# Optimization experiments

Hardware: AMD Instinct MI355X
Metric: run time of the kernel (lower is better)

Reference implementation:

```python
import jax, jax.numpy as jnp
import numpy as np

H = 8  # n_head

def rel_shift(x):
    # x: [B, H, S, 2S-1] -> [B, H, S, S]
    B, h, S, _ = x.shape
    x_padded = jnp.pad(x, ((0, 0), (0, 0), (0, 0), (1, 0)))  # [B,H,S,2S]
    x_padded = x_padded.reshape(B, h, 2 * S, S)
    x = x_padded[:, :, 1:, :].reshape(B, h, S, 2 * S - 1)
    return x[:, :, :, :S]

def setup_inputs() -> dict:
    key = jax.random.key(0)
    ks = jax.random.split(key, 16)
    B, S, D = 8, 1024, 512
    C = D // H
    inp = {
        "query": jax.random.normal(ks[0], (B, S, D), jnp.float32),
        "key": jax.random.normal(ks[1], (B, S, D), jnp.float32),
        "value": jax.random.normal(ks[2], (B, S, D), jnp.float32),
        "pos_emb": jax.random.normal(ks[3], (1, 2 * S - 1, D), jnp.float32),
        "mask": jnp.zeros((B, S), dtype=bool),
        "Wq": jax.random.normal(ks[4], (D, D), jnp.float32) / np.sqrt(D),
        "bq": jnp.zeros((D,), jnp.float32),
        "Wk": jax.random.normal(ks[5], (D, D), jnp.float32) / np.sqrt(D),
        "bk": jnp.zeros((D,), jnp.float32),
        "Wv": jax.random.normal(ks[6], (D, D), jnp.float32) / np.sqrt(D),
        "bv": jnp.zeros((D,), jnp.float32),
        "Wpos": jax.random.normal(ks[7], (D, D), jnp.float32) / np.sqrt(D),
        "Wout": jax.random.normal(ks[8], (D, D), jnp.float32) / np.sqrt(D),
        "bout": jnp.zeros((D,), jnp.float32),
        "u_bias": jax.random.normal(ks[9], (H, C), jnp.float32) / np.sqrt(C),
        "v_bias": jax.random.normal(ks[10], (H, C), jnp.float32) / np.sqrt(C),
    }
    return inp

def reference(query, key, value, pos_emb, mask, Wq, bq, Wk, bk, Wv, bv,
              Wpos, Wout, bout, u_bias, v_bias):
    B, S, D = query.shape
    C = D // H
    # qkv projections -> [B, H, S, C]
    q = (query @ Wq + bq).reshape(B, S, H, C).transpose(0, 2, 1, 3)
    k = (key @ Wk + bk).reshape(B, S, H, C).transpose(0, 2, 1, 3)
    v = (value @ Wv + bv).reshape(B, S, H, C).transpose(0, 2, 1, 3)
    # positional projection: pos_emb [1, 2S-1, D] -> p [H, 2S-1, C]
    P = pos_emb.shape[1]
    p = (pos_emb[0] @ Wpos).reshape(P, H, C).transpose(1, 0, 2)
    q_u = q + u_bias[:, None, :]
    q_v = q + v_bias[:, None, :]
    matrix_ac = jnp.einsum('bhsc,bhtc->bhst', q_u, k)           # [B,H,S,S]
    matrix_bd = jnp.einsum('bhsc,htc->bhst', q_v, p)            # [B,H,S,2S-1]
    matrix_bd = rel_shift(matrix_bd)                            # [B,H,S,S]
    scores = (matrix_ac + matrix_bd) / jnp.sqrt(jnp.float32(C))
    scores = jnp.where(mask[:, None, None, :], -jnp.inf, scores)
    p_attn = jax.nn.softmax(scores, axis=-1)
    x = jnp.einsum('bhst,bhtc->bhsc', p_attn, v)
    x = x.transpose(0, 2, 1, 3).reshape(B, S, D)
    return x @ Wout + bout
```

## Files before the change

### kernel.cpp

```cpp
#include <hip/hip_runtime.h>
#include <math.h>

typedef unsigned short ushort_t;
typedef __attribute__((ext_vector_type(8))) short short8;
typedef __attribute__((ext_vector_type(4))) float f32x4;

#define MFMA(a,b,c) __builtin_amdgcn_mfma_f32_16x16x32_bf16((a),(b),(c),0,0,0)

#define BB 8
#define SS 1024
#define DD 512
#define HH 8
#define CC 64
#define PP 2047

static __device__ __forceinline__ ushort_t f2bf(float f) {
    unsigned u = __float_as_uint(f);
    u += 0x7fffu + ((u >> 16) & 1u);
    return (ushort_t)(u >> 16);
}
static __device__ __forceinline__ unsigned pack2(float a, float b) {
    return (unsigned)f2bf(a) | ((unsigned)f2bf(b) << 16);
}

__global__ __launch_bounds__(256) void wtrans_kernel(
    const float* __restrict__ Wq, const float* __restrict__ Wk,
    const float* __restrict__ Wv, const float* __restrict__ Wp,
    const float* __restrict__ Wo, ushort_t* __restrict__ wt)
{
    __shared__ float T[64][65];
    const int bid = blockIdx.x, tid = threadIdx.x;
    const int wi   = bid >> 6;
    const int tile = bid & 63;
    const float* Wsrc = (wi == 0) ? Wq : (wi == 1) ? Wk : (wi == 2) ? Wv
                      : (wi == 3) ? Wp : Wo;
    ushort_t* Wdst = wt + (size_t)wi * 262144;
    const int tk0 = (tile >> 3) * 64, tn0 = (tile & 7) * 64;
    const int r = tid >> 2, c4 = (tid & 3) * 16;
    #pragma unroll
    for (int rep = 0; rep < 4; ++rep) {
        float4 f = *(const float4*)(Wsrc + (size_t)(tk0 + r) * 512 + tn0 + c4 + rep * 4);
        T[r][c4 + rep * 4 + 0] = f.x; T[r][c4 + rep * 4 + 1] = f.y;
        T[r][c4 + rep * 4 + 2] = f.z; T[r][c4 + rep * 4 + 3] = f.w;
    }
    __syncthreads();
    #pragma unroll
    for (int rep = 0; rep < 4; ++rep) {
        uint2 u;
        u.x = pack2(T[c4 + rep * 4 + 0][r], T[c4 + rep * 4 + 1][r]);
        u.y = pack2(T[c4 + rep * 4 + 2][r], T[c4 + rep * 4 + 3][r]);
        *(uint2*)(Wdst + (size_t)(tn0 + r) * 512 + tk0 + c4 + rep * 4) = u;
    }
}

__global__ __launch_bounds__(256) void qkvpos_kernel(
    const float* __restrict__ Xq, const float* __restrict__ Xk,
    const float* __restrict__ Xv, const float* __restrict__ Xp,
    const ushort_t* __restrict__ wt,
    const float* __restrict__ bq, const float* __restrict__ bk,
    const float* __restrict__ bv,
    const float* __restrict__ ub, const float* __restrict__ vbias,
    ushort_t* __restrict__ qu, ushort_t* __restrict__ qvo,
    ushort_t* __restrict__ kbuf, ushort_t* __restrict__ vtb,
    ushort_t* __restrict__ pbuf)
{
    __shared__ __align__(16) ushort_t Xs[128][72];
    __shared__ __align__(16) ushort_t Ws[128][72];
    const int tid = threadIdx.x;
    const int wave = tid >> 6, lane = tid & 63, quad = lane >> 4, l16 = lane & 15;
    const int bid = blockIdx.x;
    const int n0 = (bid & 3) * 128;
    const int mt = bid >> 2;
    int mode, mtl;
    if (mt < 64)       { mode = 0; mtl = mt; }
    else if (mt < 128) { mode = 1; mtl = mt - 64; }
    else if (mt < 192) { mode = 2; mtl = mt - 128; }
    else               { mode = 3; mtl = mt - 192; }
    const int m0 = mtl * 128;
    const float* X = (mode == 0) ? Xq : (mode == 1) ? Xk : (mode == 2) ? Xv : Xp;
    const ushort_t* W = wt + (size_t)mode * 262144;
    const int mb = (wave >> 1) * 64, nb = (wave & 1) * 64;

    f32x4 acc[4][4];
    #pragma unroll
    for (int i = 0; i < 4; ++i)
        #pragma unroll
        for (int j = 0; j < 4; ++j) acc[i][j] = (f32x4){0.f, 0.f, 0.f, 0.f};

    for (int k0 = 0; k0 < 512; k0 += 64) {
        #pragma unroll
        for (int i = 0; i < 4; ++i) {
            int u = tid + 256 * i; int r = u >> 3; int c8 = (u & 7) * 8;
            int row = m0 + r;
            if (mode == 3 && row > PP - 1) row = PP - 1;
            const float* xp = X + (size_t)row * 512 + k0 + c8;
            float4 fa = *(const float4*)xp;
            float4 fb = *(const float4*)(xp + 4);
            uint4 pk;
            pk.x = pack2(fa.x, fa.y); pk.y = pack2(fa.z, fa.w);
            pk.z = pack2(fb.x, fb.y); pk.w = pack2(fb.z, fb.w);
            *(uint4*)&Xs[r][c8] = pk;
            *(uint4*)&Ws[r][c8] = *(const uint4*)(W + (size_t)(n0 + r) * 512 + k0 + c8);
        }
        __syncthreads();
        #pragma unroll
        for (int kk = 0; kk < 2; ++kk) {
            short8 av[4], bv4[4];
            #pragma unroll
            for (int ms = 0; ms < 4; ++ms)
                av[ms] = *(const short8*)&Xs[mb + ms * 16 + l16][kk * 32 + quad * 8];
            #pragma unroll
            for (int ns = 0; ns < 4; ++ns)
                bv4[ns] = *(const short8*)&Ws[nb + ns * 16 + l16][kk * 32 + quad * 8];
            #pragma unroll
            for (int ms = 0; ms < 4; ++ms)
                #pragma unroll
                for (int ns = 0; ns < 4; ++ns)
                    acc[ms][ns] = MFMA(av[ms], bv4[ns], acc[ms][ns]);
        }
        __syncthreads();
    }

    #pragma unroll
    for (int ms = 0; ms < 4; ++ms)
    #pragma unroll
    for (int ns = 0; ns < 4; ++ns)
    #pragma unroll
    for (int r = 0; r < 4; ++r) {
        const int row = m0 + mb + ms * 16 + quad * 4 + r;
        const int col = n0 + nb + ns * 16 + l16;
        const float v = acc[ms][ns][r];
        if (mode == 0) {
            float base = v + bq[col];
            size_t idx = (((size_t)(row >> 10) * HH + (col >> 6)) * SS + (row & 1023)) * CC + (col & 63);
            qu[idx]  = f2bf(base + ub[col]);
            qvo[idx] = f2bf(base + vbias[col]);
        } else if (mode == 1) {
            size_t idx = (((size_t)(row >> 10) * HH + (col >> 6)) * SS + (row & 1023)) * CC + (col & 63);
            kbuf[idx] = f2bf(v + bk[col]);
        } else if (mode == 2) {
            size_t idx = (((size_t)(row >> 10) * HH + (col >> 6)) * CC + (col & 63)) * SS + (row & 1023);
            vtb[idx] = f2bf(v + bv[col]);
        } else {
            if (row < PP)
                pbuf[((size_t)(col >> 6) * PP + row) * CC + (col & 63)] = f2bf(v);
        }
    }
}

__global__ __launch_bounds__(256) void outproj_kernel(
    const ushort_t* __restrict__ X, const ushort_t* __restrict__ W,
    const float* __restrict__ b1, float* __restrict__ Yf)
{
    __shared__ __align__(16) ushort_t Xs[128][72];
    __shared__ __align__(16) ushort_t Ws[128][72];
    const int tid = threadIdx.x;
    const int wave = tid >> 6, lane = tid & 63, quad = lane >> 4, l16 = lane & 15;
    const int n0 = blockIdx.x * 128, m0 = blockIdx.y * 128;
    const int mb = (wave >> 1) * 64, nb = (wave & 1) * 64;

    f32x4 acc[4][4];
    #pragma unroll
    for (int i = 0; i < 4; ++i)
        #pragma unroll
        for (int j = 0; j < 4; ++j) acc[i][j] = (f32x4){0.f, 0.f, 0.f, 0.f};

    for (int k0 = 0; k0 < 512; k0 += 64) {
        #pragma unroll
        for (int i = 0; i < 4; ++i) {
            int u = tid + 256 * i; int r = u >> 3; int c8 = (u & 7) * 8;
            *(uint4*)&Xs[r][c8] = *(const uint4*)(X + (size_t)(m0 + r) * 512 + k0 + c8);
            *(uint4*)&Ws[r][c8] = *(const uint4*)(W + (size_t)(n0 + r) * 512 + k0 + c8);
        }
        __syncthreads();
        #pragma unroll
        for (int kk = 0; kk < 2; ++kk) {
            short8 av[4], bv4[4];
            #pragma unroll
            for (int ms = 0; ms < 4; ++ms)
                av[ms] = *(const short8*)&Xs[mb + ms * 16 + l16][kk * 32 + quad * 8];
            #pragma unroll
            for (int ns = 0; ns < 4; ++ns)
                bv4[ns] = *(const short8*)&Ws[nb + ns * 16 + l16][kk * 32 + quad * 8];
            #pragma unroll
            for (int ms = 0; ms < 4; ++ms)
                #pragma unroll
                for (int ns = 0; ns < 4; ++ns)
                    acc[ms][ns] = MFMA(av[ms], bv4[ns], acc[ms][ns]);
        }
        __syncthreads();
    }

    #pragma unroll
    for (int ms = 0; ms < 4; ++ms)
    #pragma unroll
    for (int ns = 0; ns < 4; ++ns)
    #pragma unroll
    for (int r = 0; r < 4; ++r) {
        const int row = m0 + mb + ms * 16 + quad * 4 + r;
        const int col = n0 + nb + ns * 16 + l16;
        Yf[(size_t)row * 512 + col] = acc[ms][ns][r] + b1[col];
    }
}

__global__ __launch_bounds__(512) void attn_kernel(
    const ushort_t* __restrict__ qu_g, const ushort_t* __restrict__ qv_g,
    const ushort_t* __restrict__ kb, const ushort_t* __restrict__ vt_g,
    const ushort_t* __restrict__ pbf, const unsigned char* __restrict__ mask,
    ushort_t* __restrict__ xg)
{
    const int bh = blockIdx.x;
    const int s0 = blockIdx.y * 128;
    const int b = bh >> 3, h = bh & 7;
    const int tid = threadIdx.x;
    const int wave = tid >> 6, lane = tid & 63, quad = lane >> 4, l16 = lane & 15;

    __shared__ __align__(16) ushort_t Ks[64][72];
    __shared__ __align__(16) ushort_t Vts[64][72];
    __shared__ __align__(16) ushort_t Pb[256][72];
    __shared__ __align__(16) ushort_t Pscr[8][16][72];

    const size_t qoff = ((size_t)bh * SS + s0 + wave * 16 + l16) * CC;
    short8 quA[2], qvA[2];
    quA[0] = *(const short8*)(qu_g + qoff + quad * 8);
    quA[1] = *(const short8*)(qu_g + qoff + 32 + quad * 8);
    qvA[0] = *(const short8*)(qv_g + qoff + quad * 8);
    qvA[1] = *(const short8*)(qv_g + qoff + 32 + quad * 8);

    f32x4 O[4];
    #pragma unroll
    for (int i = 0; i < 4; ++i) O[i] = (f32x4){0.f, 0.f, 0.f, 0.f};
    float lsum[4] = {0.f, 0.f, 0.f, 0.f};

    const ushort_t* kbase  = kb   + ((size_t)bh << 10) * CC;
    const ushort_t* vtbase = vt_g + ((size_t)bh << 6) * SS;
    const ushort_t* pbase  = pbf  + (size_t)h * PP * CC;
    const unsigned char* mbase = mask + b * SS;

    const int R0base = 896 - s0;
    const int uwread = 1008 - s0 - wave * 16;

    {
        const int r = tid >> 3, cc = (tid & 7) * 8;
        *(uint4*)&Ks[r][cc]  = *(const uint4*)(kbase + (size_t)r * CC + cc);
        *(uint4*)&Vts[r][cc] = *(const uint4*)(vtbase + (size_t)r * SS + cc);
        #pragma unroll
        for (int i = 0; i < 3; ++i) {
            int u = tid + 512 * i; int rr = u >> 3; int c2 = (u & 7) * 8;
            int gr = R0base + rr;
            int g = gr; if (g < 0) g = 0; if (g > PP - 1) g = PP - 1;
            *(uint4*)&Pb[gr & 255][c2] = *(const uint4*)(pbase + (size_t)g * CC + c2);
        }
    }
    __syncthreads();

    for (int t0 = 0; t0 < SS; t0 += 64) {
        const bool more = (t0 + 64) < SS;
        uint4 kp, vp, pp;
        const int r = tid >> 3, cc = (tid & 7) * 8;
        if (more) {
            kp = *(const uint4*)(kbase + (size_t)(t0 + 64 + r) * CC + cc);
            vp = *(const uint4*)(vtbase + (size_t)r * SS + t0 + 64 + cc);
            int g = R0base + t0 + 192 + r;
            if (g > PP - 1) g = PP - 1;
            pp = *(const uint4*)(pbase + (size_t)g * CC + cc);
        }

        f32x4 ac[4];
        #pragma unroll
        for (int ns = 0; ns < 4; ++ns) {
            ac[ns] = (f32x4){0.f, 0.f, 0.f, 0.f};
            #pragma unroll
            for (int kk = 0; kk < 2; ++kk) {
                short8 kf = *(const short8*)&Ks[ns * 16 + l16][kk * 32 + quad * 8];
                ac[ns] = MFMA(quA[kk], kf, ac[ns]);
            }
        }
        f32x4 bd[5];
        #pragma unroll
        for (int us = 0; us < 5; ++us) {
            bd[us] = (f32x4){0.f, 0.f, 0.f, 0.f};
            #pragma unroll
            for (int kk = 0; kk < 2; ++kk) {
                short8 pf = *(const short8*)&Pb[(uwread + t0 + us * 16 + l16) & 255][kk * 32 + quad * 8];
                bd[us] = MFMA(qvA[kk], pf, bd[us]);
            }
        }

        bool mk[4];
        #pragma unroll
        for (int ns = 0; ns < 4; ++ns) mk[ns] = mbase[t0 + ns * 16 + l16] != 0;

        float pvv[4][4];
        #pragma unroll
        for (int rr = 0; rr < 4; ++rr) {
            const int sl = quad * 4 + rr;
            const int d = l16 + 15 - sl;
            const int srcl = quad * 16 + (d & 15);
            const bool use_hi = d >= 16;
            #pragma unroll
            for (int ns = 0; ns < 4; ++ns) {
                float lo = __shfl(bd[ns][rr], srcl, 64);
                float hi = __shfl(bd[ns + 1][rr], srcl, 64);
                float bdv = use_hi ? hi : lo;
                float p = __expf((ac[ns][rr] + bdv) * 0.125f - 40.f);
                p = mk[ns] ? 0.f : p;
                pvv[ns][rr] = p;
                lsum[rr] += p;
            }
        }

        #pragma unroll
        for (int ns = 0; ns < 4; ++ns)
            #pragma unroll
            for (int rr = 0; rr < 4; ++rr)
                Pscr[wave][quad * 4 + rr][ns * 16 + l16] = f2bf(pvv[ns][rr]);
        short8 pA0 = *(const short8*)&Pscr[wave][l16][quad * 8];
        short8 pA1 = *(const short8*)&Pscr[wave][l16][32 + quad * 8];

        #pragma unroll
        for (int ns = 0; ns < 4; ++ns) {
            short8 v0 = *(const short8*)&Vts[ns * 16 + l16][quad * 8];
            short8 v1 = *(const short8*)&Vts[ns * 16 + l16][32 + quad * 8];
            O[ns] = MFMA(pA0, v0, O[ns]);
            O[ns] = MFMA(pA1, v1, O[ns]);
        }

        if (more) {
            __syncthreads();
            *(uint4*)&Ks[r][cc]  = kp;
            *(uint4*)&Vts[r][cc] = vp;
            *(uint4*)&Pb[(R0base + t0 + 192 + r) & 255][cc] = pp;
            __syncthreads();
        }
    }

    #pragma unroll
    for (int rr = 0; rr < 4; ++rr) {
        float s = lsum[rr];
        s += __shfl_xor(s, 1, 64); s += __shfl_xor(s, 2, 64);
        s += __shfl_xor(s, 4, 64); s += __shfl_xor(s, 8, 64);
        const float inv = 1.0f / s;
        #pragma unroll
        for (int ns = 0; ns < 4; ++ns)
            Pscr[wave][quad * 4 + rr][ns * 16 + l16] = f2bf(O[ns][rr] * inv);
    }
    {
        const ushort_t* src = &Pscr[wave][lane >> 2][(lane & 3) * 16];
        uint4 u0 = *(const uint4*)src;
        uint4 u1 = *(const uint4*)(src + 8);
        const int srow = s0 + wave * 16 + (lane >> 2);
        ushort_t* dst = xg + ((size_t)b * SS + srow) * DD + h * CC + (lane & 3) * 16;
        *(uint4*)dst = u0;
        *(uint4*)(dst + 8) = u1;
    }
}

extern "C" void kernel_launch(void* const* d_in, const int* in_sizes, int n_in,
                              void* d_out, int out_size, void* d_ws, size_t ws_size,
                              hipStream_t stream)
{
    (void)in_sizes; (void)n_in; (void)out_size; (void)ws_size;

    const float* query = (const float*)d_in[0];
    const float* key_  = (const float*)d_in[1];
    const float* value = (const float*)d_in[2];
    const float* pos   = (const float*)d_in[3];
    const unsigned char* mask = (const unsigned char*)d_in[4];
    const float* Wq   = (const float*)d_in[5];
    const float* bq   = (const float*)d_in[6];
    const float* Wk   = (const float*)d_in[7];
    const float* bk   = (const float*)d_in[8];
    const float* Wv   = (const float*)d_in[9];
    const float* bv   = (const float*)d_in[10];
    const float* Wpos = (const float*)d_in[11];
    const float* Wout = (const float*)d_in[12];
    const float* bout = (const float*)d_in[13];
    const float* ub   = (const float*)d_in[14];
    const float* vb   = (const float*)d_in[15];

    const size_t NBS = (size_t)BB * SS * DD;
    const size_t NP  = (size_t)PP * DD;
    const size_t NW  = (size_t)DD * DD;

    ushort_t* wt   = (ushort_t*)d_ws;
    ushort_t* qu   = wt + 5 * NW;
    ushort_t* qv   = qu + NBS;
    ushort_t* kbuf = qv + NBS;
    ushort_t* vtb  = kbuf + NBS;
    ushort_t* pbuf = vtb + NBS;
    ushort_t* xg   = pbuf + NP;

    ushort_t* WtO = wt + 4 * NW;

    wtrans_kernel<<<dim3(320), dim3(256), 0, stream>>>(Wq, Wk, Wv, Wpos, Wout, wt);

    qkvpos_kernel<<<dim3(832), dim3(256), 0, stream>>>(
        query, key_, value, pos, wt, bq, bk, bv, ub, vb,
        qu, qv, kbuf, vtb, pbuf);

    attn_kernel<<<dim3(64, 8), dim3(512), 0, stream>>>(qu, qv, kbuf, vtb, pbuf, mask, xg);

    outproj_kernel<<<dim3(4, 64), dim3(256), 0, stream>>>(xg, WtO, bout, (float*)d_out);
}
```

Measured before the change: 247.7 us.

## Shrink projection GEMM tiles, swizzle block order, stage epilogue through LDS for vector stores

```diff
diff --git a/kernel.cpp b/kernel.cpp
--- a/kernel.cpp
+++ b/kernel.cpp
@@ -64,87 +64,141 @@
     ushort_t* __restrict__ kbuf, ushort_t* __restrict__ vtb,
     ushort_t* __restrict__ pbuf)
 {
-    __shared__ __align__(16) ushort_t Xs[128][72];
-    __shared__ __align__(16) ushort_t Ws[128][72];
+    __shared__ __align__(16) ushort_t smem[64 * 72 + 128 * 72];
+    ushort_t (*Xs)[72] = (ushort_t(*)[72])smem;
+    ushort_t (*Ws)[72] = (ushort_t(*)[72])(smem + 64 * 72);
+    ushort_t (*Es)[136] = (ushort_t(*)[136])smem;
+    ushort_t (*EsT)[72] = (ushort_t(*)[72])smem;
+
     const int tid = threadIdx.x;
     const int wave = tid >> 6, lane = tid & 63, quad = lane >> 4, l16 = lane & 15;
     const int bid = blockIdx.x;
-    const int n0 = (bid & 3) * 128;
-    const int mt = bid >> 2;
+    const int nt = (bid >> 3) & 3;
+    const int mt = (bid & 7) + 8 * (bid >> 5);
+    const int n0 = nt * 128;
     int mode, mtl;
-    if (mt < 64)       { mode = 0; mtl = mt; }
-    else if (mt < 128) { mode = 1; mtl = mt - 64; }
-    else if (mt < 192) { mode = 2; mtl = mt - 128; }
-    else               { mode = 3; mtl = mt - 192; }
-    const int m0 = mtl * 128;
+    if (mt < 128)      { mode = 0; mtl = mt; }
+    else if (mt < 256) { mode = 1; mtl = mt - 128; }
+    else if (mt < 384) { mode = 2; mtl = mt - 256; }
+    else               { mode = 3; mtl = mt - 384; }
+    const int m0 = mtl * 64;
     const float* X = (mode == 0) ? Xq : (mode == 1) ? Xk : (mode == 2) ? Xv : Xp;
     const ushort_t* W = wt + (size_t)mode * 262144;
-    const int mb = (wave >> 1) * 64, nb = (wave & 1) * 64;
-
-    f32x4 acc[4][4];
+
+    f32x4 acc[4][2];
     #pragma unroll
     for (int i = 0; i < 4; ++i)
         #pragma unroll
-        for (int j = 0; j < 4; ++j) acc[i][j] = (f32x4){0.f, 0.f, 0.f, 0.f};
-
+        for (int j = 0; j < 2; ++j) acc[i][j] = (f32x4){0.f, 0.f, 0.f, 0.f};
+
+    const int xr = tid >> 2, xc = (tid & 3) * 16;
     for (int k0 = 0; k0 < 512; k0 += 64) {
-        #pragma unroll
-        for (int i = 0; i < 4; ++i) {
-            int u = tid + 256 * i; int r = u >> 3; int c8 = (u & 7) * 8;
-            int row = m0 + r;
+        {
+            int row = m0 + xr;
             if (mode == 3 && row > PP - 1) row = PP - 1;
-            const float* xp = X + (size_t)row * 512 + k0 + c8;
-            float4 fa = *(const float4*)xp;
-            float4 fb = *(const float4*)(xp + 4);
-            uint4 pk;
-            pk.x = pack2(fa.x, fa.y); pk.y = pack2(fa.z, fa.w);
-            pk.z = pack2(fb.x, fb.y); pk.w = pack2(fb.z, fb.w);
-            *(uint4*)&Xs[r][c8] = pk;
-            *(uint4*)&Ws[r][c8] = *(const uint4*)(W + (size_t)(n0 + r) * 512 + k0 + c8);
+            const float* xp = X + (size_t)row * 512 + k0 + xc;
+            float4 f0 = *(const float4*)xp;
+            float4 f1 = *(const float4*)(xp + 4);
+            float4 f2 = *(const float4*)(xp + 8);
+            float4 f3 = *(const float4*)(xp + 12);
+            uint4 a, bpk;
+            a.x = pack2(f0.x, f0.y); a.y = pack2(f0.z, f0.w);
+            a.z = pack2(f1.x, f1.y); a.w = pack2(f1.z, f1.w);
+            bpk.x = pack2(f2.x, f2.y); bpk.y = pack2(f2.z, f2.w);
+            bpk.z = pack2(f3.x, f3.y); bpk.w = pack2(f3.z, f3.w);
+            *(uint4*)&Xs[xr][xc] = a;
+            *(uint4*)&Xs[xr][xc + 8] = bpk;
+            #pragma unroll
+            for (int i = 0; i < 2; ++i) {
+                int u = tid + 256 * i;
+                int r = u >> 2, cc = (u & 3) * 16;
+                const ushort_t* wp = W + (size_t)(n0 + r) * 512 + k0 + cc;
+                *(uint4*)&Ws[r][cc]     = *(const uint4*)wp;
+                *(uint4*)&Ws[r][cc + 8] = *(const uint4*)(wp + 8);
+            }
         }
         __syncthreads();
         #pragma unroll
         for (int kk = 0; kk < 2; ++kk) {
-            short8 av[4], bv4[4];
+            short8 av[4], bv4[2];
             #pragma unroll
             for (int ms = 0; ms < 4; ++ms)
-                av[ms] = *(const short8*)&Xs[mb + ms * 16 + l16][kk * 32 + quad * 8];
-            #pragma unroll
-            for (int ns = 0; ns < 4; ++ns)
-                bv4[ns] = *(const short8*)&Ws[nb + ns * 16 + l16][kk * 32 + quad * 8];
+                av[ms] = *(const short8*)&Xs[ms * 16 + l16][kk * 32 + quad * 8];
+            #pragma unroll
+            for (int ns = 0; ns < 2; ++ns)
+                bv4[ns] = *(const short8*)&Ws[wave * 32 + ns * 16 + l16][kk * 32 + quad * 8];
             #pragma unroll
             for (int ms = 0; ms < 4; ++ms)
                 #pragma unroll
-                for (int ns = 0; ns < 4; ++ns)
+                for (int ns = 0; ns < 2; ++ns)
                     acc[ms][ns] = MFMA(av[ms], bv4[ns], acc[ms][ns]);
         }
         __syncthreads();
     }
 
-    #pragma unroll
-    for (int ms = 0; ms < 4; ++ms)
-    #pragma unroll
-    for (int ns = 0; ns < 4; ++ns)
-    #pragma unroll
-    for (int r = 0; r < 4; ++r) {
-        const int row = m0 + mb + ms * 16 + quad * 4 + r;
-        const int col = n0 + nb + ns * 16 + l16;
-        const float v = acc[ms][ns][r];
-        if (mode == 0) {
-            float base = v + bq[col];
-            size_t idx = (((size_t)(row >> 10) * HH + (col >> 6)) * SS + (row & 1023)) * CC + (col & 63);
-            qu[idx]  = f2bf(base + ub[col]);
-            qvo[idx] = f2bf(base + vbias[col]);
-        } else if (mode == 1) {
-            size_t idx = (((size_t)(row >> 10) * HH + (col >> 6)) * SS + (row & 1023)) * CC + (col & 63);
-            kbuf[idx] = f2bf(v + bk[col]);
-        } else if (mode == 2) {
-            size_t idx = (((size_t)(row >> 10) * HH + (col >> 6)) * CC + (col & 63)) * SS + (row & 1023);
-            vtb[idx] = f2bf(v + bv[col]);
+    float b1c[2], b2c[2], b3c[2];
+    #pragma unroll
+    for (int ns = 0; ns < 2; ++ns) {
+        const int gcol = n0 + wave * 32 + ns * 16 + l16;
+        if (mode == 0) { b1c[ns] = bq[gcol]; b2c[ns] = ub[gcol]; b3c[ns] = vbias[gcol]; }
+        else if (mode == 1) { b1c[ns] = bk[gcol]; }
+        else if (mode == 2) { b1c[ns] = bv[gcol]; }
+        else b1c[ns] = 0.f;
+    }
+
+    const int npass = (mode == 0) ? 2 : 1;
+    for (int pass = 0; pass < npass; ++pass) {
+        #pragma unroll
+        for (int ms = 0; ms < 4; ++ms)
+        #pragma unroll
+        for (int ns = 0; ns < 2; ++ns)
+        #pragma unroll
+        for (int r = 0; r < 4; ++r) {
+            const int lrow = ms * 16 + quad * 4 + r;
+            const int lcol = wave * 32 + ns * 16 + l16;
+            float v = acc[ms][ns][r];
+            if (mode == 0) v += b1c[ns] + (pass == 0 ? b2c[ns] : b3c[ns]);
+            else if (mode != 3) v += b1c[ns];
+            if (mode == 2) EsT[lcol][lrow] = f2bf(v);
+            else           Es[lrow][lcol]  = f2bf(v);
+        }
+        __syncthreads();
+        if (mode == 2) {
+            const int b = m0 >> 10;
+            #pragma unroll
+            for (int i = 0; i < 4; ++i) {
+                int u = tid + 256 * i;
+                int cl = u >> 3, off8 = (u & 7) * 8;
+                uint4 d = *(const uint4*)&EsT[cl][off8];
+                const int gcol = n0 + cl;
+                ushort_t* dst = vtb + (((size_t)(b * HH + (gcol >> 6))) * CC + (gcol & 63)) * SS
+                                + (m0 & 1023) + off8;
+                *(uint4*)dst = d;
+            }
         } else {
-            if (row < PP)
-                pbuf[((size_t)(col >> 6) * PP + row) * CC + (col & 63)] = f2bf(v);
-        }
+            #pragma unroll
+            for (int i = 0; i < 4; ++i) {
+                int u = tid + 256 * i;
+                int seg = u >> 3, off8 = (u & 7) * 8;
+                int sl = seg >> 1, hsel = seg & 1;
+                int lc = hsel * 64 + off8;
+                uint4 d = *(const uint4*)&Es[sl][lc];
+                const int grow = m0 + sl;
+                const int gcol = n0 + lc;
+                if (mode == 3) {
+                    if (grow < PP) {
+                        ushort_t* dst = pbuf + ((size_t)(gcol >> 6) * PP + grow) * CC + (gcol & 63);
+                        *(uint4*)dst = d;
+                    }
+                } else {
+                    size_t idx = (((size_t)(grow >> 10) * HH + (gcol >> 6)) * SS + (grow & 1023)) * CC + (gcol & 63);
+                    ushort_t* dst = (mode == 1) ? (kbuf + idx)
+                                  : (pass == 0 ? (qu + idx) : (qvo + idx));
+                    *(uint4*)dst = d;
+                }
+            }
+        }
+        if (pass + 1 < npass) __syncthreads();
     }
 }
 
@@ -152,40 +206,52 @@
     const ushort_t* __restrict__ X, const ushort_t* __restrict__ W,
     const float* __restrict__ b1, float* __restrict__ Yf)
 {
-    __shared__ __align__(16) ushort_t Xs[128][72];
-    __shared__ __align__(16) ushort_t Ws[128][72];
+    __shared__ __align__(16) ushort_t smem[64 * 72 + 128 * 72];
+    ushort_t (*Xs)[72] = (ushort_t(*)[72])smem;
+    ushort_t (*Ws)[72] = (ushort_t(*)[72])(smem + 64 * 72);
+
     const int tid = threadIdx.x;
     const int wave = tid >> 6, lane = tid & 63, quad = lane >> 4, l16 = lane & 15;
-    const int n0 = blockIdx.x * 128, m0 = blockIdx.y * 128;
-    const int mb = (wave >> 1) * 64, nb = (wave & 1) * 64;
-
-    f32x4 acc[4][4];
+    const int bid = blockIdx.x;
+    const int nt = (bid >> 3) & 3;
+    const int mtl = (bid & 7) + 8 * (bid >> 5);
+    const int n0 = nt * 128, m0 = mtl * 64;
+
+    f32x4 acc[4][2];
     #pragma unroll
     for (int i = 0; i < 4; ++i)
         #pragma unroll
-        for (int j = 0; j < 4; ++j) acc[i][j] = (f32x4){0.f, 0.f, 0.f, 0.f};
-
+        for (int j = 0; j < 2; ++j) acc[i][j] = (f32x4){0.f, 0.f, 0.f, 0.f};
+
+    const int xr = tid >> 2, xc = (tid & 3) * 16;
     for (int k0 = 0; k0 < 512; k0 += 64) {
-        #pragma unroll
-        for (int i = 0; i < 4; ++i) {
-            int u = tid + 256 * i; int r = u >> 3; int c8 = (u & 7) * 8;
-            *(uint4*)&Xs[r][c8] = *(const uint4*)(X + (size_t)(m0 + r) * 512 + k0 + c8);
-            *(uint4*)&Ws[r][c8] = *(const uint4*)(W + (size_t)(n0 + r) * 512 + k0 + c8);
+        {
+            const ushort_t* xp = X + (size_t)(m0 + xr) * 512 + k0 + xc;
+            *(uint4*)&Xs[xr][xc]     = *(const uint4*)xp;
+            *(uint4*)&Xs[xr][xc + 8] = *(const uint4*)(xp + 8);
+            #pragma unroll
+            for (int i = 0; i < 2; ++i) {
+                int u = tid + 256 * i;
+                int r = u >> 2, cc = (u & 3) * 16;
+                const ushort_t* wp = W + (size_t)(n0 + r) * 512 + k0 + cc;
+                *(uint4*)&Ws[r][cc]     = *(const uint4*)wp;
+                *(uint4*)&Ws[r][cc + 8] = *(const uint4*)(wp + 8);
+            }
         }
         __syncthreads();
         #pragma unroll
         for (int kk = 0; kk < 2; ++kk) {
-            short8 av[4], bv4[4];
+            short8 av[4], bv4[2];
             #pragma unroll
             for (int ms = 0; ms < 4; ++ms)
-                av[ms] = *(const short8*)&Xs[mb + ms * 16 + l16][kk * 32 + quad * 8];
-            #pragma unroll
-            for (int ns = 0; ns < 4; ++ns)
-                bv4[ns] = *(const short8*)&Ws[nb + ns * 16 + l16][kk * 32 + quad * 8];
+                av[ms] = *(const short8*)&Xs[ms * 16 + l16][kk * 32 + quad * 8];
+            #pragma unroll
+            for (int ns = 0; ns < 2; ++ns)
+                bv4[ns] = *(const short8*)&Ws[wave * 32 + ns * 16 + l16][kk * 32 + quad * 8];
             #pragma unroll
             for (int ms = 0; ms < 4; ++ms)
                 #pragma unroll
-                for (int ns = 0; ns < 4; ++ns)
+                for (int ns = 0; ns < 2; ++ns)
                     acc[ms][ns] = MFMA(av[ms], bv4[ns], acc[ms][ns]);
         }
         __syncthreads();
@@ -194,11 +260,11 @@
     #pragma unroll
     for (int ms = 0; ms < 4; ++ms)
     #pragma unroll
-    for (int ns = 0; ns < 4; ++ns)
+    for (int ns = 0; ns < 2; ++ns)
     #pragma unroll
     for (int r = 0; r < 4; ++r) {
-        const int row = m0 + mb + ms * 16 + quad * 4 + r;
-        const int col = n0 + nb + ns * 16 + l16;
+        const int row = m0 + ms * 16 + quad * 4 + r;
+        const int col = n0 + wave * 32 + ns * 16 + l16;
         Yf[(size_t)row * 512 + col] = acc[ms][ns][r] + b1[col];
     }
 }
@@ -395,11 +461,11 @@
 
     wtrans_kernel<<<dim3(320), dim3(256), 0, stream>>>(Wq, Wk, Wv, Wpos, Wout, wt);
 
-    qkvpos_kernel<<<dim3(832), dim3(256), 0, stream>>>(
+    qkvpos_kernel<<<dim3(1664), dim3(256), 0, stream>>>(
         query, key_, value, pos, wt, bq, bk, bv, ub, vb,
         qu, qv, kbuf, vtb, pbuf);
 
     attn_kernel<<<dim3(64, 8), dim3(512), 0, stream>>>(qu, qv, kbuf, vtb, pbuf, mask, xg);
 
-    outproj_kernel<<<dim3(4, 64), dim3(256), 0, stream>>>(xg, WtO, bout, (float*)d_out);
-}
+    outproj_kernel<<<dim3(512), dim3(256), 0, stream>>>(xg, WtO, bout, (float*)d_out);
+}
```

Result: faster. 237.3 us (-4.2%).
